# Performance work log

Hardware: AMD Instinct MI355X
Metric: run time of the kernel (lower is better)

The kernel has to match this reference:

```python
import jax, jax.numpy as jnp
import numpy as np

TOPK = 5
LAMBDA_ALIGN_K = 16.0
MOM = 0.9          # EMA momentum
DEFAULT_SCORE = 0.5  # EMA bank default (bank starts empty)
EPS = 1e-8
NEG = 1.0e9


def pairwise_cosine(X):
    # torch F.normalize: X / max(||X||, eps)
    n = jnp.linalg.norm(X, axis=-1, keepdims=True)
    Xn = X / jnp.maximum(n, EPS)
    sim = Xn @ Xn.T
    return jnp.clip(sim, -1.0 + EPS, 1.0 - EPS)


def knn_mask(sim, allowed_base, topk=TOPK):
    B = sim.shape[0]
    eye = jnp.eye(B, dtype=sim.dtype)
    allowed = allowed_base * (1.0 - eye)
    masked = sim - NEG * eye
    masked = jnp.where(allowed < 0.5, -NEG, masked)
    masked = jnp.where(masked < 0.0, -NEG, masked)
    cand = (masked > 0).sum(axis=1)
    k = min(topk, max(B - 1, 1))
    keep_row = (cand >= topk).astype(sim.dtype)
    keep = keep_row[:, None] * keep_row[None, :]
    idx = jax.lax.top_k(masked, k)[1]                       # [B, k]
    M = jnp.zeros_like(sim).at[jnp.arange(B)[:, None], idx].set(1.0)
    M = jnp.maximum(M, M.T)
    return M * allowed * keep


def build_intra(sim, same, topk=TOPK):
    M = knn_mask(sim, same, topk)
    A = jnp.maximum(sim * M, 0.0) * same
    return A, M


def pga_loss(feats_sub, labels_sub):
    # feats_sub: [L, b, d]
    L = feats_sub.shape[0]
    same = (labels_sub[:, None] == labels_sub[None, :]).astype(jnp.float32)
    sims = jax.vmap(pairwise_cosine)(feats_sub)             # [L, b, b]
    A, M = jax.vmap(lambda s: build_intra(s, same))(sims)   # [L, b, b] each

    # EMA degree-based scores (no-grad in original; bank starts empty so
    # fetch-after-update == mom*default + (1-mom)*score_cur)
    S_intra = jnp.maximum(sims * same, 0.0)
    deg = jnp.maximum((S_intra > 0).sum(axis=2).astype(jnp.float32), 1.0)
    score_cur = jax.nn.sigmoid(S_intra.sum(axis=2) / deg)   # [L, b]
    ema = jax.lax.stop_gradient(MOM * DEFAULT_SCORE + (1.0 - MOM) * score_cur)

    # layer-pair masked MSE alignment, target detached
    A_deep = A[1:]
    A_tgt = jax.lax.stop_gradient(A[:-1])
    M_eff = jnp.maximum(M[:-1], M[1:])                      # [L-1, b, b]
    W = ema[:-1, :, None] * ema[:-1, None, :]               # [L-1, b, b]
    diff2 = (A_deep - A_tgt) ** 2 * W
    num = (diff2 * M_eff).sum(axis=(1, 2))
    den = jnp.maximum((M_eff * W).sum(axis=(1, 2)), EPS)
    terms = jnp.where(M_eff.sum(axis=(1, 2)) > 0, num / den, 0.0)
    raw = terms.sum() / max(L - 1, 1)
    return LAMBDA_ALIGN_K * raw


def setup_inputs() -> dict:
    key = jax.random.key(0)
    k1, k2 = jax.random.split(key)
    feats_final = jax.random.normal(k1, (8, 2048, 512), dtype=jnp.float32)
    labels = jax.random.randint(k2, (2048,), 0, 128).astype(jnp.int64)
    sample_ids = jnp.arange(2048, dtype=jnp.int64)
    return {"feats_final": feats_final, "labels": labels, "sample_ids": sample_ids}


def reference(feats_final, labels, sample_ids):
    # candidate subset from last layer (no-grad in original)
    X_last = feats_final[-1]
    S_last = pairwise_cosine(X_last)
    same_full = (labels[:, None] == labels[None, :]).astype(jnp.float32)
    _, M_last = build_intra(S_last, same_full)
    cand_mask = (M_last > 0).sum(axis=1) > 0
    idx_sub = jnp.nonzero(cand_mask)[0]  # eager (concrete) subselection
    feats_sub = feats_final[:, idx_sub]  # [L, b, d]
    labels_sub = labels[idx_sub]
    return pga_loss(feats_sub, labels_sub)
```

## Files before the change

kernel.cpp:

```cpp
#include <hip/hip_runtime.h>
#include <cmath>

#define NB   2048
#define ND   512
#define NL   8
#define NLAB 128
#define MAXM 64
#define TOPK_ 5
#define NTH  256
#define MAXSLOT 9
#define GSTRIDE (MAXM*MAXM)

__global__ __launch_bounds__(NTH) void k_gram(
    const float* __restrict__ feats, const int* __restrict__ labels,
    float* __restrict__ G, int* __restrict__ cnt,
    unsigned long long* __restrict__ insub)
{
    __shared__ int cnts[NTH];
    __shared__ int g_s[MAXM];
    __shared__ float Xt[MAXM][132];
    __shared__ float rinvp[64];
    __shared__ unsigned long long tops_s[64];
    __shared__ unsigned char keep_s[64];
    int c = blockIdx.x, l = blockIdx.y, tid = threadIdx.x;

    int my[8]; int n = 0; int base_i = tid * 8;
    for (int t = 0; t < 8; ++t) {
        int i = base_i + t;
        if (labels[i] == c) my[n++] = i;
    }
    cnts[tid] = n;
    __syncthreads();
    for (int off = 1; off < NTH; off <<= 1) {
        int v = (tid >= off) ? cnts[tid - off] : 0;
        __syncthreads();
        cnts[tid] += v;
        __syncthreads();
    }
    int excl = cnts[tid] - n;
    int m = cnts[NTH - 1]; if (m > MAXM) m = MAXM;
    for (int t = 0; t < n; ++t) {
        int slot = excl + t;
        if (slot < MAXM) g_s[slot] = my[t];
    }
    if (l == 0 && tid == 0) cnt[c] = m;
    __syncthreads();
    if (m == 0) {
        if (l == 7 && tid == 0) insub[c] = 0ull;
        return;
    }

    const float* X = feats + (size_t)l * NB * ND;
    const int P = m * (m + 1) / 2;
    float acc0[MAXSLOT], acc1[MAXSLOT];
    short is_[MAXSLOT], js_[MAXSLOT];
    int ns = 0;
    for (int p = tid; p < P; p += NTH) {
        int i = (int)((sqrtf(8.0f * (float)p + 1.0f) - 1.0f) * 0.5f);
        while (((i + 1) * (i + 2)) / 2 <= p) ++i;
        while ((i * (i + 1)) / 2 > p) --i;
        is_[ns] = (short)i;
        js_[ns] = (short)(p - (i * (i + 1)) / 2);
        acc0[ns] = 0.0f; acc1[ns] = 0.0f;
        ++ns;
    }
    for (int kc = 0; kc < ND; kc += 128) {
        if (kc) __syncthreads();
        for (int idx = tid; idx < (m << 5); idx += NTH) {
            int i = idx >> 5, k4 = idx & 31;
            float4 v = *(const float4*)(X + ((size_t)g_s[i] << 9) + kc + (k4 << 2));
            *(float4*)&Xt[i][k4 << 2] = v;
        }
        __syncthreads();
        for (int s = 0; s < ns; ++s) {
            int i = is_[s], j = js_[s];
            float a0 = acc0[s], a1 = acc1[s];
            #pragma unroll
            for (int k4 = 0; k4 < 32; ++k4) {
                float4 a = *(const float4*)&Xt[i][k4 << 2];
                float4 b = *(const float4*)&Xt[j][k4 << 2];
                a0 = fmaf(a.x, b.x, a0); a1 = fmaf(a.y, b.y, a1);
                a0 = fmaf(a.z, b.z, a0); a1 = fmaf(a.w, b.w, a1);
            }
            acc0[s] = a0; acc1[s] = a1;
        }
    }
    float* Gc = G + ((size_t)l * NLAB + c) * GSTRIDE;
    for (int s = 0; s < ns; ++s) {
        int i = is_[s], j = js_[s];
        float v = acc0[s] + acc1[s];
        Gc[i * MAXM + j] = v;
        Gc[j * MAXM + i] = v;
    }
    if (l != 7) return;

    float (*Gs)[65] = (float(*)[65])(&Xt[0][0]);
    __syncthreads();
    for (int s = 0; s < ns; ++s) {
        int i = is_[s], j = js_[s];
        float v = acc0[s] + acc1[s];
        Gs[i][j] = v; Gs[j][i] = v;
    }
    if (tid < m) for (int j = m; j < 64; ++j) Gs[tid][j] = -2.0f;
    __syncthreads();
    if (tid < 64) {
        rinvp[tid] = (tid < m) ? 1.0f / fmaxf(sqrtf(Gs[tid][tid]), 1e-8f) : 0.0f;
        keep_s[tid] = 0; tops_s[tid] = 0ull;
    }
    __syncthreads();
    unsigned long long tops = 0ull; bool keep = false;
    if (tid < m) {
        float ri = rinvp[tid];
        float v0=-1.f,v1=-1.f,v2=-1.f,v3=-1.f,v4=-1.f;
        int i0=0,i1=0,i2=0,i3=0,i4=0, cand=0;
        #pragma unroll 8
        for (int j = 0; j < 64; ++j) {
            float raw = Gs[tid][j];
            float v = fminf(fmaxf(raw * ri * rinvp[j], -1.0f), 1.0f);
            if (raw == -2.0f) v = -2.0f;
            if (v > 0.0f && j != tid) {
                ++cand;
                if      (v > v0) { v4=v3;i4=i3; v3=v2;i3=i2; v2=v1;i2=i1; v1=v0;i1=i0; v0=v;i0=j; }
                else if (v > v1) { v4=v3;i4=i3; v3=v2;i3=i2; v2=v1;i2=i1; v1=v;i1=j; }
                else if (v > v2) { v4=v3;i4=i3; v3=v2;i3=i2; v2=v;i2=j; }
                else if (v > v3) { v4=v3;i4=i3; v3=v;i3=j; }
                else if (v > v4) { v4=v;i4=j; }
            }
        }
        keep = (cand >= TOPK_);
        if (keep) tops = (1ull<<i0)|(1ull<<i1)|(1ull<<i2)|(1ull<<i3)|(1ull<<i4);
        keep_s[tid] = keep ? 1 : 0; tops_s[tid] = tops;
    }
    __syncthreads();
    unsigned long long Mrow = 0ull;
    if (tid < m && keep) {
        for (int j = 0; j < 64; ++j) {
            if (j == tid || !keep_s[j]) continue;
            if (((tops >> j) & 1ull) || ((tops_s[j] >> tid) & 1ull)) Mrow |= (1ull << j);
        }
    }
    if (tid < 64) {
        unsigned long long b = __ballot(Mrow != 0ull);
        if (tid == 0) insub[c] = b;
    }
}

__device__ __forceinline__ void load_tile(
    const float* __restrict__ Gc, int m, int tid, float (*Gs)[65], float* rinv)
{
    if (tid < 64) rinv[tid] = (tid < m) ? 1.0f / fmaxf(sqrtf(Gc[tid * MAXM + tid]), 1e-8f) : 0.0f;
    __syncthreads();
    int tot = m << 4;
    for (int idx4 = tid; idx4 < tot; idx4 += NTH) {
        int i = idx4 >> 4, j0 = (idx4 & 15) << 2;
        float4 raw = *(const float4*)(Gc + i * MAXM + j0);
        float ri = rinv[i];
        Gs[i][j0 + 0] = (j0 + 0 < m) ? fminf(fmaxf(raw.x * ri * rinv[j0 + 0], -1.0f), 1.0f) : -2.0f;
        Gs[i][j0 + 1] = (j0 + 1 < m) ? fminf(fmaxf(raw.y * ri * rinv[j0 + 1], -1.0f), 1.0f) : -2.0f;
        Gs[i][j0 + 2] = (j0 + 2 < m) ? fminf(fmaxf(raw.z * ri * rinv[j0 + 2], -1.0f), 1.0f) : -2.0f;
        Gs[i][j0 + 3] = (j0 + 3 < m) ? fminf(fmaxf(raw.w * ri * rinv[j0 + 3], -1.0f), 1.0f) : -2.0f;
    }
    __syncthreads();
}

__global__ __launch_bounds__(NTH) void k_decide(
    const float* __restrict__ G, const int* __restrict__ cnt,
    const unsigned long long* __restrict__ insub,
    unsigned long long* __restrict__ Mbits, float* __restrict__ ema)
{
    __shared__ float Gs[64][65];
    __shared__ float rinv[64];
    __shared__ unsigned long long tops_s[64];
    __shared__ unsigned char keep_s[64];
    int c = blockIdx.x, l = blockIdx.y, tid = threadIdx.x;
    int m = cnt[c]; if (m > MAXM) m = MAXM;
    if (m == 0) return;
    unsigned long long sub = insub[c];

    const float* Gc = G + ((size_t)l * NLAB + c) * GSTRIDE;
    load_tile(Gc, m, tid, Gs, rinv);
    if (tid < 64) { keep_s[tid] = 0; tops_s[tid] = 0ull; }
    __syncthreads();
    unsigned long long tops = 0ull; bool keep = false; bool act = false;
    float emaval = 0.0f;
    if (tid < m) {
        act = (sub >> tid) & 1ull;
        if (act) {
            float v0=-1.f,v1=-1.f,v2=-1.f,v3=-1.f,v4=-1.f;
            int i0=0,i1=0,i2=0,i3=0,i4=0, cand=0, dg=0;
            float rs = 0.0f;
            #pragma unroll 8
            for (int j = 0; j < 64; ++j) {
                float v = Gs[tid][j];
                if (!((sub >> j) & 1ull)) v = -2.0f;
                if (v > 0.0f) {
                    rs += v; ++dg;
                    if (j != tid) {
                        ++cand;
                        if      (v > v0) { v4=v3;i4=i3; v3=v2;i3=i2; v2=v1;i2=i1; v1=v0;i1=i0; v0=v;i0=j; }
                        else if (v > v1) { v4=v3;i4=i3; v3=v2;i3=i2; v2=v1;i2=i1; v1=v;i1=j; }
                        else if (v > v2) { v4=v3;i4=i3; v3=v2;i3=i2; v2=v;i2=j; }
                        else if (v > v3) { v4=v3;i4=i3; v3=v;i3=j; }
                        else if (v > v4) { v4=v;i4=j; }
                    }
                }
            }
            keep = (cand >= TOPK_);
            if (keep) tops = (1ull<<i0)|(1ull<<i1)|(1ull<<i2)|(1ull<<i3)|(1ull<<i4);
            float deg = (float)(dg > 0 ? dg : 1);
            float score = 1.0f / (1.0f + expf(-rs / deg));
            emaval = 0.45f + 0.1f * score;
        }
        keep_s[tid] = keep ? 1 : 0; tops_s[tid] = tops;
    }
    __syncthreads();
    if (tid < m) {
        unsigned long long Mrow = 0ull;
        if (keep) {
            for (int j = 0; j < 64; ++j) {
                if (j == tid || !keep_s[j]) continue;
                if (((tops >> j) & 1ull) || ((tops_s[j] >> tid) & 1ull)) Mrow |= (1ull << j);
            }
        }
        Mbits[((size_t)l * NLAB + c) * MAXM + tid] = Mrow;
        ema[((size_t)l * NLAB + c) * MAXM + tid] = emaval;
    }
}

__global__ __launch_bounds__(NTH) void k_pairs(
    const float* __restrict__ G, const int* __restrict__ cnt,
    const unsigned long long* __restrict__ Mbits, const float* __restrict__ ema,
    float* __restrict__ partial)
{
    __shared__ float r0[64], r1[64];
    __shared__ unsigned long long M0s[64], M1s[64];
    __shared__ float es[64];
    __shared__ float red[12];
    int c = blockIdx.x, p = blockIdx.y, tid = threadIdx.x;
    int m = cnt[c]; if (m > MAXM) m = MAXM;
    const float* G0 = G + ((size_t)p       * NLAB + c) * GSTRIDE;
    const float* G1 = G + ((size_t)(p + 1) * NLAB + c) * GSTRIDE;
    if (tid < m) {
        M0s[tid] = Mbits[((size_t)p * NLAB + c) * MAXM + tid];
        M1s[tid] = Mbits[((size_t)(p + 1) * NLAB + c) * MAXM + tid];
        es[tid]  = ema[((size_t)p * NLAB + c) * MAXM + tid];
        r0[tid]  = 1.0f / fmaxf(sqrtf(G0[tid * MAXM + tid]), 1e-8f);
        r1[tid]  = 1.0f / fmaxf(sqrtf(G1[tid * MAXM + tid]), 1e-8f);
    }
    __syncthreads();
    float fn = 0.0f, fd = 0.0f, fc = 0.0f;
    for (int idx = tid; idx < (m << 6); idx += NTH) {
        int i = idx >> 6, j = idx & 63;
        if (j >= m) continue;
        bool b0 = (M0s[i] >> j) & 1ull;
        bool b1 = (M1s[i] >> j) & 1ull;
        if (b0 | b1) {
            float v0 = b0 ? fminf(fmaxf(G0[idx] * r0[i] * r0[j], -1.0f), 1.0f) : 0.0f;
            float v1 = b1 ? fminf(fmaxf(G1[idx] * r1[i] * r1[j], -1.0f), 1.0f) : 0.0f;
            float w = es[i] * es[j];
            float d = v1 - v0;
            fn = fmaf(d * d, w, fn);
            fd += w;
            fc += 1.0f;
        }
    }
    for (int off = 32; off > 0; off >>= 1) {
        fn += __shfl_down(fn, off);
        fd += __shfl_down(fd, off);
        fc += __shfl_down(fc, off);
    }
    int w = tid >> 6;
    if ((tid & 63) == 0) { red[w * 3] = fn; red[w * 3 + 1] = fd; red[w * 3 + 2] = fc; }
    __syncthreads();
    if (tid == 0) {
        float* dst = partial + ((size_t)p * NLAB + c) * 4;
        dst[0] = red[0] + red[3] + red[6] + red[9];
        dst[1] = red[1] + red[4] + red[7] + red[10];
        dst[2] = red[2] + red[5] + red[8] + red[11];
    }
}

__global__ void k_final(const float* __restrict__ partial, float* __restrict__ out)
{
    int tid = threadIdx.x;
    float total = 0.0f;
    for (int p = 0; p < NL - 1; ++p) {
        float n = 0.0f, d = 0.0f, cc = 0.0f;
        for (int c = tid; c < NLAB; c += 64) {
            const float* src = partial + ((size_t)p * NLAB + c) * 4;
            n += src[0]; d += src[1]; cc += src[2];
        }
        for (int off = 32; off > 0; off >>= 1) {
            n += __shfl_down(n, off);
            d += __shfl_down(d, off);
            cc += __shfl_down(cc, off);
        }
        if (tid == 0 && cc > 0.0f) total += n / fmaxf(d, 1e-8f);
    }
    if (tid == 0) out[0] = 16.0f * total / 7.0f;
}

extern "C" void kernel_launch(void* const* d_in, const int* in_sizes, int n_in,
                              void* d_out, int out_size, void* d_ws, size_t ws_size,
                              hipStream_t stream) {
    const float* feats  = (const float*)d_in[0];
    const int*   labels = (const int*)d_in[1];
    char* w = (char*)d_ws;
    size_t gbytes = (size_t)NL * NLAB * GSTRIDE * 4;
    float*    G       = (float*)(w);
    float*    partial = (float*)(w + gbytes);
    int*      cnt     = (int*)(w + gbytes + 14336);
    unsigned long long* insub = (unsigned long long*)(w + gbytes + 14848);
    unsigned long long* Mbits = (unsigned long long*)(w + gbytes + 16384);
    float*    ema     = (float*)(w + gbytes + 16384 + 524288);
    float*    out     = (float*)d_out;

    k_gram  <<<dim3(NLAB, NL), NTH, 0, stream>>>(feats, labels, G, cnt, insub);
    k_decide<<<dim3(NLAB, NL), NTH, 0, stream>>>(G, cnt, insub, Mbits, ema);
    k_pairs <<<dim3(NLAB, NL - 1), NTH, 0, stream>>>(G, cnt, Mbits, ema, partial);
    k_final <<<1, 64, 0, stream>>>(partial, out);
}
```

Measured before the change: 134.7 us.

## Prefetch next feature chunk into registers and use wave-shuffle prefix scan

Replaces the shared-memory block prefix scan (many barriers) with a wavefront shuffle scan plus a four-entry cross-wave combine. Global loads of the next 128-wide feature chunk are issued into registers before the dot-product loop runs, so load latency overlaps compute instead of stalling at each chunk. This costs extra registers for the prefetch buffers and row pointers, which may lower occupancy.

After: 142.0 us. 5.4% more time.

```diff
diff --git a/kernel.cpp b/kernel.cpp
--- a/kernel.cpp
+++ b/kernel.cpp
@@ -9,6 +9,7 @@
 #define TOPK_ 5
 #define NTH  256
 #define MAXSLOT 9
+#define MAXST   8
 #define GSTRIDE (MAXM*MAXM)
 
 __global__ __launch_bounds__(NTH) void k_gram(
@@ -16,29 +17,32 @@
     float* __restrict__ G, int* __restrict__ cnt,
     unsigned long long* __restrict__ insub)
 {
-    __shared__ int cnts[NTH];
+    __shared__ int wsum[4];
     __shared__ int g_s[MAXM];
     __shared__ float Xt[MAXM][132];
     __shared__ float rinvp[64];
     __shared__ unsigned long long tops_s[64];
     __shared__ unsigned char keep_s[64];
     int c = blockIdx.x, l = blockIdx.y, tid = threadIdx.x;
+    int lane = tid & 63, wv = tid >> 6;
 
     int my[8]; int n = 0; int base_i = tid * 8;
     for (int t = 0; t < 8; ++t) {
         int i = base_i + t;
         if (labels[i] == c) my[n++] = i;
     }
-    cnts[tid] = n;
-    __syncthreads();
-    for (int off = 1; off < NTH; off <<= 1) {
-        int v = (tid >= off) ? cnts[tid - off] : 0;
-        __syncthreads();
-        cnts[tid] += v;
-        __syncthreads();
-    }
-    int excl = cnts[tid] - n;
-    int m = cnts[NTH - 1]; if (m > MAXM) m = MAXM;
+    int scan = n;
+    #pragma unroll
+    for (int off = 1; off < 64; off <<= 1) {
+        int v = __shfl_up(scan, off);
+        if (lane >= off) scan += v;
+    }
+    if (lane == 63) wsum[wv] = scan;
+    __syncthreads();
+    int w0 = wsum[0], w1 = wsum[1], w2 = wsum[2], w3 = wsum[3];
+    int m = w0 + w1 + w2 + w3; if (m > MAXM) m = MAXM;
+    int base = (wv > 0 ? w0 : 0) + (wv > 1 ? w1 : 0) + (wv > 2 ? w2 : 0);
+    int excl = base + scan - n;
     for (int t = 0; t < n; ++t) {
         int slot = excl + t;
         if (slot < MAXM) g_s[slot] = my[t];
@@ -51,6 +55,18 @@
     }
 
     const float* X = feats + (size_t)l * NB * ND;
+
+    int nst = 0; short st_i[MAXST], st_k4[MAXST];
+    const float* rowp[MAXST];
+    for (int idx = tid; idx < (m << 5); idx += NTH) {
+        st_i[nst] = (short)(idx >> 5);
+        st_k4[nst] = (short)(idx & 31);
+        rowp[nst] = X + ((size_t)g_s[idx >> 5] << 9) + ((idx & 31) << 2);
+        ++nst;
+    }
+    float4 pre[MAXST];
+    for (int s = 0; s < nst; ++s) pre[s] = *(const float4*)(rowp[s]);
+
     const int P = m * (m + 1) / 2;
     float acc0[MAXSLOT], acc1[MAXSLOT];
     short is_[MAXSLOT], js_[MAXSLOT];
@@ -64,14 +80,15 @@
         acc0[ns] = 0.0f; acc1[ns] = 0.0f;
         ++ns;
     }
+
     for (int kc = 0; kc < ND; kc += 128) {
         if (kc) __syncthreads();
-        for (int idx = tid; idx < (m << 5); idx += NTH) {
-            int i = idx >> 5, k4 = idx & 31;
-            float4 v = *(const float4*)(X + ((size_t)g_s[i] << 9) + kc + (k4 << 2));
-            *(float4*)&Xt[i][k4 << 2] = v;
-        }
+        for (int s = 0; s < nst; ++s)
+            *(float4*)&Xt[st_i[s]][st_k4[s] << 2] = pre[s];
         __syncthreads();
+        if (kc + 128 < ND)
+            for (int s = 0; s < nst; ++s)
+                pre[s] = *(const float4*)(rowp[s] + kc + 128);
         for (int s = 0; s < ns; ++s) {
             int i = is_[s], j = js_[s];
             float a0 = acc0[s], a1 = acc1[s];
```
